# Optimization experiments

Hardware: AMD Instinct MI355X
Metric: run time of the kernel (lower is better)

The kernel has to match this reference:

```python
import jax, jax.numpy as jnp
import numpy as np

N, E, F, H = 50000, 800000, 256, 64


def setup_inputs() -> dict:
    key = jax.random.key(0)
    ks = jax.random.split(key, 6)
    x = jax.random.normal(ks[0], (N, F), jnp.float32)
    edge_index = jax.random.randint(ks[1], (2, E), 0, N)
    init = lambda k, shp, fan: jax.random.normal(k, shp, jnp.float32) / np.float32(np.sqrt(fan))
    W1l = init(ks[2], (F, H), F)
    b1l = jnp.zeros((H,), jnp.float32)
    W1r = init(ks[3], (F, H), F)
    W2l = init(ks[4], (H, H), H)
    b2l = jnp.zeros((H,), jnp.float32)
    W2r = init(ks[5], (H, H), H)
    return dict(x=x, edge_index=edge_index, W1l=W1l, b1l=b1l, W1r=W1r,
                W2l=W2l, b2l=b2l, W2r=W2r)


def _sage(x, src, dst, Wl, bl, Wr, n):
    # SAGEConv: out = mean_{j->i}(lin_l(x)_j) + lin_r(x)_i
    m = x @ Wl + bl                                   # [N, H]
    agg = jax.ops.segment_sum(m[src], dst, num_segments=n)
    deg = jax.ops.segment_sum(jnp.ones((src.shape[0],), x.dtype), dst, num_segments=n)
    agg = agg / jnp.maximum(deg, 1.0)[:, None]        # mean aggregation
    return agg + x @ Wr


def reference(x, edge_index, W1l, b1l, W1r, W2l, b2l, W2r):
    src, dst = edge_index[0], edge_index[1]
    n = x.shape[0]
    # 2-layer SAGE encoder (dropout=0, no residual for 2 layers)
    h = jax.nn.relu(_sage(x, src, dst, W1l, b1l, W1r, n))
    z = _sage(h, src, dst, W2l, b2l, W2r, n)
    # UnitNorm: replace all-zero rows with randn, then row-wise L2 normalize
    valid = jnp.sum(z != 0, axis=1, keepdims=True) > 0
    r = jax.random.normal(jax.random.key(42), z.shape, z.dtype)
    z = jnp.where(valid, z, r)
    z = z / jnp.sqrt(jnp.sum(z * z, axis=1, keepdims=True))
    # dot-product decode on observed edges + positive-edge BCE loss
    scores = jnp.sum(z[src] * z[dst], axis=-1)        # [E]
    loss = -jnp.mean(jax.nn.log_sigmoid(scores))
    return z, loss
```

## Files before the change

### kernel.cpp

```cpp
#include <hip/hip_runtime.h>

#define N_NODES 50000
#define N_EDGES 800000
#define F_IN    256
#define H_DIM   64
#define NB_SCAN ((N_NODES + 255) / 256)
#define TILE_A  4096
#define EPT     (TILE_A / 256)
#define MAXB    5632

typedef __attribute__((ext_vector_type(8))) short short8;
typedef __attribute__((ext_vector_type(4))) float floatx4;

__device__ __forceinline__ unsigned short f2bf(float f) {
  unsigned int u;
  __builtin_memcpy(&u, &f, 4);
  u += 0x7fffu + ((u >> 16) & 1u);
  return (unsigned short)(u >> 16);
}
__device__ __forceinline__ float bf2f(unsigned short s) {
  unsigned int v = ((unsigned int)s) << 16; float f; __builtin_memcpy(&f, &v, 4); return f;
}
__device__ __forceinline__ float bflo(unsigned int u) {
  unsigned int v = u << 16; float f; __builtin_memcpy(&f, &v, 4); return f;
}
__device__ __forceinline__ float bfhi(unsigned int u) {
  unsigned int v = u & 0xffff0000u; float f; __builtin_memcpy(&f, &v, 4); return f;
}

template<int K>
__device__ __forceinline__ void pack_body(int t, const float* __restrict__ Wl,
                                          const float* __restrict__ Wr,
                                          unsigned short* __restrict__ Wb)
{
  int lane = t & 63;
  int f    = t >> 6;
  int m    = f & 1;
  int c    = (f >> 1) & 3;
  int ks   = f >> 3;
  const float* W = m ? Wr : Wl;
  int quad = lane >> 4, l15 = lane & 15;
  int col = c * 16 + l15;
  unsigned short u[8];
#pragma unroll
  for (int j = 0; j < 8; ++j) {
    int k = ks * 32 + quad * 8 + j;
    u[j] = f2bf(W[k * H_DIM + col]);
  }
  uint4 v;
  __builtin_memcpy(&v, u, 16);
  ((uint4*)Wb)[t] = v;
}

__global__ __launch_bounds__(256) void pack_all_k(
    const float* __restrict__ W1l, const float* __restrict__ W1r,
    const float* __restrict__ W2l, const float* __restrict__ W2r,
    unsigned short* __restrict__ Wb1, unsigned short* __restrict__ Wb2,
    float* __restrict__ loss_slot, int* __restrict__ bcur)
{
  if (blockIdx.x == 0) {
    if (threadIdx.x == 0) loss_slot[0] = 0.f;
    if (threadIdx.x < NB_SCAN) bcur[threadIdx.x] = 0;
  }
  int b = blockIdx.x;
  if (b < 16) {
    pack_body<F_IN>(b * 256 + threadIdx.x, W1l, W1r, Wb1);
  } else {
    pack_body<H_DIM>((b - 16) * 256 + threadIdx.x, W2l, W2r, Wb2);
  }
}

template<int K, bool XBF16>
__global__ __launch_bounds__(256, 4) void gemm_mfma_k(
    const void* __restrict__ X_,
    const unsigned short* __restrict__ Wb,
    const float* __restrict__ bl,
    unsigned short* __restrict__ outl, unsigned short* __restrict__ outr)
{
  constexpr int KP = K + 8;
  __shared__ unsigned short xs[64 * KP];
  const int row0 = blockIdx.x * 64;
  if (XBF16) {
    const uint4* X = (const uint4*)X_;
    const int CH = K / 8;
    for (int i = threadIdx.x; i < 64 * CH; i += 256) {
      int r = i / CH, c = i % CH;
      int row = row0 + r;
      uint4 v = (row < N_NODES) ? X[(size_t)row * CH + c] : make_uint4(0, 0, 0, 0);
      *(uint4*)&xs[r * KP + c * 8] = v;
    }
  } else {
    const float4* X = (const float4*)X_;
    const int CH = K / 4;
    for (int i = threadIdx.x; i < 64 * CH; i += 256) {
      int r = i / CH, c = i % CH;
      int row = row0 + r;
      float4 v = (row < N_NODES) ? X[(size_t)row * CH + c]
                                 : make_float4(0.f, 0.f, 0.f, 0.f);
      unsigned int lo = (unsigned int)f2bf(v.x) | ((unsigned int)f2bf(v.y) << 16);
      unsigned int hi = (unsigned int)f2bf(v.z) | ((unsigned int)f2bf(v.w) << 16);
      *(uint2*)&xs[r * KP + c * 4] = make_uint2(lo, hi);
    }
  }
  __syncthreads();

  const int lane = threadIdx.x & 63;
  const int w    = threadIdx.x >> 6;
  const int quad = lane >> 4;
  const int l15  = lane & 15;
  const int rloc = w * 16 + l15;

  floatx4 accl[4], accr[4];
#pragma unroll
  for (int c = 0; c < 4; ++c) { accl[c] = (floatx4)0.f; accr[c] = (floatx4)0.f; }

  const uint4* wbase = (const uint4*)Wb;
#pragma unroll
  for (int ks = 0; ks < K / 32; ++ks) {
    short8 af = *(const short8*)&xs[rloc * KP + ks * 32 + quad * 8];
#pragma unroll
    for (int c = 0; c < 4; ++c) {
      uint4 rl = wbase[((ks * 4 + c) * 2 + 0) * 64 + lane];
      uint4 rr = wbase[((ks * 4 + c) * 2 + 1) * 64 + lane];
      short8 bfl, bfr;
      __builtin_memcpy(&bfl, &rl, 16);
      __builtin_memcpy(&bfr, &rr, 16);
      accl[c] = __builtin_amdgcn_mfma_f32_16x16x32_bf16(af, bfl, accl[c], 0, 0, 0);
      accr[c] = __builtin_amdgcn_mfma_f32_16x16x32_bf16(af, bfr, accr[c], 0, 0, 0);
    }
  }
#pragma unroll
  for (int c = 0; c < 4; ++c) {
    int col = c * 16 + l15;
    float bias = bl[col];
#pragma unroll
    for (int reg = 0; reg < 4; ++reg) {
      int row = row0 + w * 16 + quad * 4 + reg;
      if (row < N_NODES) {
        outl[(size_t)row * H_DIM + col] = f2bf(accl[c][reg] + bias);
        outr[(size_t)row * H_DIM + col] = f2bf(accr[c][reg]);
      }
    }
  }
}

__global__ __launch_bounds__(256) void binA_k(const int* __restrict__ ei,
                                              int* __restrict__ bcur,
                                              unsigned int* __restrict__ ebuf)
{
  __shared__ int lcnt[256];
  __shared__ int lofs[256];
  __shared__ int lstart[256];
  __shared__ int gstart[256];
  __shared__ int lcur[256];
  __shared__ unsigned int ldata[TILE_A];
  const int t = threadIdx.x;
  const int e0 = blockIdx.x * TILE_A;
  lcnt[t] = 0;
  __syncthreads();
  int ss[EPT], ds[EPT];
#pragma unroll
  for (int j = 0; j < EPT; ++j) {
    int e = e0 + t + j * 256;
    if (e < N_EDGES) {
      ss[j] = ei[e];
      ds[j] = ei[N_EDGES + e];
      atomicAdd(&lcnt[ds[j] >> 8], 1);
    } else {
      ds[j] = -1;
    }
  }
  __syncthreads();
  int v = lcnt[t];
  lofs[t] = v;
  __syncthreads();
  for (int off = 1; off < 256; off <<= 1) {
    int u = (t >= off) ? lofs[t - off] : 0;
    __syncthreads();
    lofs[t] += u;
    __syncthreads();
  }
  lstart[t] = lofs[t] - v;
  lcur[t]   = lofs[t] - v;
  if (t < NB_SCAN && v > 0) gstart[t] = atomicAdd(&bcur[t], v);
  __syncthreads();
#pragma unroll
  for (int j = 0; j < EPT; ++j) {
    if (ds[j] >= 0) {
      int p = atomicAdd(&lcur[ds[j] >> 8], 1);
      ldata[p] = ((unsigned int)ss[j] << 8) | (unsigned int)(ds[j] & 255);
    }
  }
  __syncthreads();
  int w = t >> 6, lane = t & 63;
  for (int b = w; b < NB_SCAN; b += 4) {
    int st = lstart[b], len = lcnt[b];
    if (len == 0) continue;
    int g = gstart[b];
    unsigned int* dst = ebuf + (size_t)b * MAXB;
    for (int j = lane; j < len; j += 64) {
      int gp = g + j;
      if (gp < MAXB) dst[gp] = ldata[st + j];
    }
  }
}

__global__ __launch_bounds__(256) void binB_k(const unsigned int* __restrict__ ebuf,
                                              const int* __restrict__ bcur,
                                              int* __restrict__ esrc,
                                              int* __restrict__ edst,
                                              int* __restrict__ rowptr)
{
  __shared__ int sc[256];
  __shared__ int ncnt[256];
  __shared__ int nscan[256];
  __shared__ int ncur[256];
  __shared__ int sh_se[2];
  __shared__ unsigned int sdata[MAXB];
  const int b = blockIdx.x, t = threadIdx.x;
  int bl = (t < NB_SCAN) ? min(bcur[t], MAXB) : 0;
  sc[t] = bl;
  __syncthreads();
  for (int off = 1; off < 256; off <<= 1) {
    int u = (t >= off) ? sc[t - off] : 0;
    __syncthreads();
    sc[t] += u;
    __syncthreads();
  }
  if (t == b) { sh_se[0] = sc[t] - bl; sh_se[1] = bl; }
  __syncthreads();
  const int start = sh_se[0], len = sh_se[1];
  const unsigned int* eb = ebuf + (size_t)b * MAXB;
  ncnt[t] = 0;
  __syncthreads();
  for (int i = t; i < len; i += 256) atomicAdd(&ncnt[eb[i] & 255], 1);
  __syncthreads();
  int v = ncnt[t];
  nscan[t] = v;
  __syncthreads();
  for (int off = 1; off < 256; off <<= 1) {
    int u = (t >= off) ? nscan[t - off] : 0;
    __syncthreads();
    nscan[t] += u;
    __syncthreads();
  }
  ncur[t] = nscan[t] - v;
  __syncthreads();
  for (int i = t; i < len; i += 256) {
    unsigned int e = eb[i];
    int p = atomicAdd(&ncur[e & 255], 1);
    sdata[p] = e >> 8;
  }
  __syncthreads();
  for (int i = t; i < len; i += 256) esrc[start + i] = (int)sdata[i];
  int node = b * 256 + t;
  int s0 = start + nscan[t] - v;
  if (node < N_NODES) {
    rowptr[node] = s0;
    if (node == N_NODES - 1) rowptr[N_NODES] = s0 + v;
  }
  for (int j = 0; j < v; ++j) edst[s0 + j] = node;
}

__device__ __forceinline__ float agg_row_b(const int* __restrict__ esrc,
                                           const unsigned short* __restrict__ m,
                                           int b, int e, int lane)
{
  float a0 = 0.f, a1 = 0.f, a2 = 0.f, a3 = 0.f;
  float a4 = 0.f, a5 = 0.f, a6 = 0.f, a7 = 0.f;
  int i = b;
  for (; i + 8 <= e; i += 8) {
    int s0 = esrc[i],     s1 = esrc[i + 1], s2 = esrc[i + 2], s3 = esrc[i + 3];
    int s4 = esrc[i + 4], s5 = esrc[i + 5], s6 = esrc[i + 6], s7 = esrc[i + 7];
    a0 += bf2f(m[(size_t)s0 * H_DIM + lane]);
    a1 += bf2f(m[(size_t)s1 * H_DIM + lane]);
    a2 += bf2f(m[(size_t)s2 * H_DIM + lane]);
    a3 += bf2f(m[(size_t)s3 * H_DIM + lane]);
    a4 += bf2f(m[(size_t)s4 * H_DIM + lane]);
    a5 += bf2f(m[(size_t)s5 * H_DIM + lane]);
    a6 += bf2f(m[(size_t)s6 * H_DIM + lane]);
    a7 += bf2f(m[(size_t)s7 * H_DIM + lane]);
  }
  for (; i + 4 <= e; i += 4) {
    int s0 = esrc[i], s1 = esrc[i + 1], s2 = esrc[i + 2], s3 = esrc[i + 3];
    a0 += bf2f(m[(size_t)s0 * H_DIM + lane]);
    a1 += bf2f(m[(size_t)s1 * H_DIM + lane]);
    a2 += bf2f(m[(size_t)s2 * H_DIM + lane]);
    a3 += bf2f(m[(size_t)s3 * H_DIM + lane]);
  }
  for (; i < e; ++i) a0 += bf2f(m[(size_t)esrc[i] * H_DIM + lane]);
  return ((a0 + a1) + (a2 + a3)) + ((a4 + a5) + (a6 + a7));
}

__global__ __launch_bounds__(256) void agg1_k(
    const int* __restrict__ rowptr, const int* __restrict__ esrc,
    const unsigned short* __restrict__ m, const unsigned short* __restrict__ xr,
    unsigned short* __restrict__ h)
{
  int gid = blockIdx.x * 256 + threadIdx.x;
  int row = gid >> 6, lane = gid & 63;
  if (row >= N_NODES) return;
  int b = rowptr[row], e = rowptr[row + 1];
  float acc = agg_row_b(esrc, m, b, e, lane);
  float dv = fmaxf((float)(e - b), 1.f);
  size_t o = (size_t)row * H_DIM + lane;
  h[o] = f2bf(fmaxf(acc / dv + bf2f(xr[o]), 0.f));
}

__global__ __launch_bounds__(256) void agg2_k(
    const int* __restrict__ rowptr, const int* __restrict__ esrc,
    const unsigned short* __restrict__ m, const unsigned short* __restrict__ hr,
    float* __restrict__ zout, unsigned short* __restrict__ zb)
{
  int gid = blockIdx.x * 256 + threadIdx.x;
  int row = gid >> 6, lane = gid & 63;
  if (row >= N_NODES) return;
  int b = rowptr[row], e = rowptr[row + 1];
  float acc = agg_row_b(esrc, m, b, e, lane);
  float dv = fmaxf((float)(e - b), 1.f);
  size_t o = (size_t)row * H_DIM + lane;
  float v = acc / dv + bf2f(hr[o]);
  float ss = v * v;
#pragma unroll
  for (int mm = 32; mm >= 1; mm >>= 1) ss += __shfl_xor(ss, mm, 64);
  float z = v * rsqrtf(fmaxf(ss, 1e-30f));
  zout[o] = z;
  zb[o] = f2bf(z);
}

__global__ __launch_bounds__(256) void decode2_k(
    const int* __restrict__ esrc, const int* __restrict__ edst,
    const unsigned short* __restrict__ zb, float* __restrict__ loss_slot)
{
  int i0 = (blockIdx.x * 256 + threadIdx.x) * 2;
  float part = 0.f;
  if (i0 + 1 < N_EDGES) {
    int s0 = esrc[i0],     d0 = edst[i0];
    int s1 = esrc[i0 + 1], d1 = edst[i0 + 1];
    const uint4* zs0 = (const uint4*)(zb + (size_t)s0 * H_DIM);
    const uint4* zd0 = (const uint4*)(zb + (size_t)d0 * H_DIM);
    const uint4* zs1 = (const uint4*)(zb + (size_t)s1 * H_DIM);
    const uint4* zd1 = (const uint4*)(zb + (size_t)d1 * H_DIM);
    float p0 = 0.f, p1 = 0.f;
#pragma unroll 4
    for (int k = 0; k < 8; ++k) {
      uint4 a0 = zs0[k], b0 = zd0[k], a1 = zs1[k], b1 = zd1[k];
      unsigned int au0[4] = {a0.x, a0.y, a0.z, a0.w};
      unsigned int bu0[4] = {b0.x, b0.y, b0.z, b0.w};
      unsigned int au1[4] = {a1.x, a1.y, a1.z, a1.w};
      unsigned int bu1[4] = {b1.x, b1.y, b1.z, b1.w};
#pragma unroll
      for (int j = 0; j < 4; ++j) {
        p0 = fmaf(bflo(au0[j]), bflo(bu0[j]), p0);
        p0 = fmaf(bfhi(au0[j]), bfhi(bu0[j]), p0);
        p1 = fmaf(bflo(au1[j]), bflo(bu1[j]), p1);
        p1 = fmaf(bfhi(au1[j]), bfhi(bu1[j]), p1);
      }
    }
    part  = fmaxf(-p0, 0.f) + log1pf(expf(-fabsf(p0)));
    part += fmaxf(-p1, 0.f) + log1pf(expf(-fabsf(p1)));
  }
#pragma unroll
  for (int m = 32; m >= 1; m >>= 1) part += __shfl_xor(part, m, 64);
  __shared__ float sbuf[4];
  int lane = threadIdx.x & 63, w = threadIdx.x >> 6;
  if (lane == 0) sbuf[w] = part;
  __syncthreads();
  if (threadIdx.x == 0)
    atomicAdd(loss_slot, (sbuf[0] + sbuf[1] + sbuf[2] + sbuf[3]) * (1.0f / N_EDGES));
}

extern "C" void kernel_launch(void* const* d_in, const int* in_sizes, int n_in,
                              void* d_out, int out_size, void* d_ws, size_t ws_size,
                              hipStream_t stream)
{
  (void)in_sizes; (void)n_in; (void)out_size; (void)ws_size;
  const float* x   = (const float*)d_in[0];
  const int*   ei  = (const int*)d_in[1];
  const float* W1l = (const float*)d_in[2];
  const float* b1l = (const float*)d_in[3];
  const float* W1r = (const float*)d_in[4];
  const float* W2l = (const float*)d_in[5];
  const float* b2l = (const float*)d_in[6];
  const float* W2r = (const float*)d_in[7];
  float* out = (float*)d_out;
  float* loss_slot = out + (size_t)N_NODES * H_DIM;

  const size_t NH = (size_t)N_NODES * H_DIM;
  unsigned short* uA = (unsigned short*)d_ws;
  unsigned short* uB = uA + NH;
  unsigned short* uC = uB + NH;
  unsigned short* Wb1 = uC + NH;
  unsigned short* Wb2 = Wb1 + (F_IN / 32) * 4 * 2 * 64 * 8;
  int* rowptr = (int*)(Wb2 + (H_DIM / 32) * 4 * 2 * 64 * 8);
  int* esrc   = rowptr + N_NODES + 1;
  int* edst   = esrc + N_EDGES;
  int* bcur   = edst + N_EDGES;
  unsigned int* ebuf = (unsigned int*)(bcur + NB_SCAN);

  dim3 blk(256);
  dim3 g_tile((N_NODES + 63) / 64);
  dim3 g_edge2((N_EDGES / 2 + 255) / 256);
  dim3 g_node((N_NODES * 64 + 255) / 256);
  dim3 g_binA((N_EDGES + TILE_A - 1) / TILE_A);
  dim3 g_bin(NB_SCAN);

  pack_all_k<<<dim3(20), blk, 0, stream>>>(W1l, W1r, W2l, W2r, Wb1, Wb2,
                                           loss_slot, bcur);
  binA_k<<<g_binA, blk, 0, stream>>>(ei, bcur, ebuf);
  binB_k<<<g_bin, blk, 0, stream>>>(ebuf, bcur, esrc, edst, rowptr);
  gemm_mfma_k<F_IN, false><<<g_tile, blk, 0, stream>>>(x, Wb1, b1l, uA, uC);
  agg1_k<<<g_node, blk, 0, stream>>>(rowptr, esrc, uA, uC, uB);
  gemm_mfma_k<H_DIM, true><<<g_tile, blk, 0, stream>>>(uB, Wb2, b2l, uA, uC);
  agg2_k<<<g_node, blk, 0, stream>>>(rowptr, esrc, uA, uC, out, uB);
  decode2_k<<<g_edge2, blk, 0, stream>>>(esrc, edst, uB, loss_slot);
}
```

Measured before the change: 254.5 us.

## Fuse binB into gemm1 launch and decode loss over CSR rows without edst

Merges the CSR bin-sort stage and the first-layer GEMM into one launch, with blocks split by index and sharing one shared-memory buffer, so the independent work overlaps and a launch is saved. The edge decode now walks CSR rows with one wavefront per destination node. Each destination row of z is loaded once per wavefront and every neighbour dot product is reduced with wave shuffles, which removes the edst array and its writes in binB. The trade-offs are per-edge shuffle reductions and load imbalance across rows of different degree in the decode. The fused kernel's shared-memory size follows the larger GEMM tile, which may limit occupancy for the binB blocks.

```diff
diff --git a/kernel.cpp b/kernel.cpp
--- a/kernel.cpp
+++ b/kernel.cpp
@@ -8,6 +8,8 @@
 #define TILE_A  4096
 #define EPT     (TILE_A / 256)
 #define MAXB    5632
+#define GT1     ((N_NODES + 63) / 64)
+#define DEC_BLOCKS 1568
 
 typedef __attribute__((ext_vector_type(8))) short short8;
 typedef __attribute__((ext_vector_type(4))) float floatx4;
@@ -20,12 +22,6 @@
 }
 __device__ __forceinline__ float bf2f(unsigned short s) {
   unsigned int v = ((unsigned int)s) << 16; float f; __builtin_memcpy(&f, &v, 4); return f;
-}
-__device__ __forceinline__ float bflo(unsigned int u) {
-  unsigned int v = u << 16; float f; __builtin_memcpy(&f, &v, 4); return f;
-}
-__device__ __forceinline__ float bfhi(unsigned int u) {
-  unsigned int v = u & 0xffff0000u; float f; __builtin_memcpy(&f, &v, 4); return f;
 }
 
 template<int K>
@@ -71,15 +67,15 @@
 }
 
 template<int K, bool XBF16>
-__global__ __launch_bounds__(256, 4) void gemm_mfma_k(
+__device__ __forceinline__ void gemm_body(
+    int bx, unsigned short* xs,
     const void* __restrict__ X_,
     const unsigned short* __restrict__ Wb,
     const float* __restrict__ bl,
     unsigned short* __restrict__ outl, unsigned short* __restrict__ outr)
 {
   constexpr int KP = K + 8;
-  __shared__ unsigned short xs[64 * KP];
-  const int row0 = blockIdx.x * 64;
+  const int row0 = bx * 64;
   if (XBF16) {
     const uint4* X = (const uint4*)X_;
     const int CH = K / 8;
@@ -205,19 +201,18 @@
   }
 }
 
-__global__ __launch_bounds__(256) void binB_k(const unsigned int* __restrict__ ebuf,
-                                              const int* __restrict__ bcur,
-                                              int* __restrict__ esrc,
-                                              int* __restrict__ edst,
-                                              int* __restrict__ rowptr)
-{
-  __shared__ int sc[256];
-  __shared__ int ncnt[256];
-  __shared__ int nscan[256];
-  __shared__ int ncur[256];
-  __shared__ int sh_se[2];
-  __shared__ unsigned int sdata[MAXB];
-  const int b = blockIdx.x, t = threadIdx.x;
+__device__ __forceinline__ void binB_body(
+    int b, unsigned char* smem,
+    const unsigned int* __restrict__ ebuf, const int* __restrict__ bcur,
+    int* __restrict__ esrc, int* __restrict__ rowptr)
+{
+  int* sc    = (int*)smem;
+  int* ncnt  = sc + 256;
+  int* nscan = ncnt + 256;
+  int* ncur  = nscan + 256;
+  int* sh_se = ncur + 256;
+  unsigned int* sdata = (unsigned int*)(sh_se + 2);
+  const int t = threadIdx.x;
   int bl = (t < NB_SCAN) ? min(bcur[t], MAXB) : 0;
   sc[t] = bl;
   __syncthreads();
@@ -259,7 +254,30 @@
     rowptr[node] = s0;
     if (node == N_NODES - 1) rowptr[N_NODES] = s0 + v;
   }
-  for (int j = 0; j < v; ++j) edst[s0 + j] = node;
+}
+
+__global__ __launch_bounds__(256, 4) void binB_gemm1_k(
+    const float* __restrict__ x, const unsigned short* __restrict__ Wb1,
+    const float* __restrict__ b1l,
+    unsigned short* __restrict__ m1, unsigned short* __restrict__ xr,
+    const unsigned int* __restrict__ ebuf, const int* __restrict__ bcur,
+    int* __restrict__ esrc, int* __restrict__ rowptr)
+{
+  __shared__ __align__(16) unsigned char smem[64 * (F_IN + 8) * 2];
+  if (blockIdx.x < GT1) {
+    gemm_body<F_IN, false>(blockIdx.x, (unsigned short*)smem, x, Wb1, b1l, m1, xr);
+  } else {
+    binB_body(blockIdx.x - GT1, smem, ebuf, bcur, esrc, rowptr);
+  }
+}
+
+__global__ __launch_bounds__(256, 4) void gemm2_k(
+    const void* __restrict__ X_, const unsigned short* __restrict__ Wb,
+    const float* __restrict__ bl,
+    unsigned short* __restrict__ outl, unsigned short* __restrict__ outr)
+{
+  __shared__ __align__(16) unsigned short xs[64 * (H_DIM + 8)];
+  gemm_body<H_DIM, true>(blockIdx.x, xs, X_, Wb, bl, outl, outr);
 }
 
 __device__ __forceinline__ float agg_row_b(const int* __restrict__ esrc,
@@ -328,42 +346,41 @@
   zb[o] = f2bf(z);
 }
 
-__global__ __launch_bounds__(256) void decode2_k(
-    const int* __restrict__ esrc, const int* __restrict__ edst,
+__global__ __launch_bounds__(256) void decode_csr_k(
+    const int* __restrict__ rowptr, const int* __restrict__ esrc,
     const unsigned short* __restrict__ zb, float* __restrict__ loss_slot)
 {
-  int i0 = (blockIdx.x * 256 + threadIdx.x) * 2;
+  const int lane = threadIdx.x & 63;
+  const int wid  = (blockIdx.x * 256 + threadIdx.x) >> 6;
+  const int nw   = DEC_BLOCKS * 4;
   float part = 0.f;
-  if (i0 + 1 < N_EDGES) {
-    int s0 = esrc[i0],     d0 = edst[i0];
-    int s1 = esrc[i0 + 1], d1 = edst[i0 + 1];
-    const uint4* zs0 = (const uint4*)(zb + (size_t)s0 * H_DIM);
-    const uint4* zd0 = (const uint4*)(zb + (size_t)d0 * H_DIM);
-    const uint4* zs1 = (const uint4*)(zb + (size_t)s1 * H_DIM);
-    const uint4* zd1 = (const uint4*)(zb + (size_t)d1 * H_DIM);
-    float p0 = 0.f, p1 = 0.f;
-#pragma unroll 4
-    for (int k = 0; k < 8; ++k) {
-      uint4 a0 = zs0[k], b0 = zd0[k], a1 = zs1[k], b1 = zd1[k];
-      unsigned int au0[4] = {a0.x, a0.y, a0.z, a0.w};
-      unsigned int bu0[4] = {b0.x, b0.y, b0.z, b0.w};
-      unsigned int au1[4] = {a1.x, a1.y, a1.z, a1.w};
-      unsigned int bu1[4] = {b1.x, b1.y, b1.z, b1.w};
-#pragma unroll
-      for (int j = 0; j < 4; ++j) {
-        p0 = fmaf(bflo(au0[j]), bflo(bu0[j]), p0);
-        p0 = fmaf(bfhi(au0[j]), bfhi(bu0[j]), p0);
-        p1 = fmaf(bflo(au1[j]), bflo(bu1[j]), p1);
-        p1 = fmaf(bfhi(au1[j]), bfhi(bu1[j]), p1);
+  for (int row = wid; row < N_NODES; row += nw) {
+    int b = rowptr[row], e = rowptr[row + 1];
+    if (b == e) continue;
+    float zd = bf2f(zb[(size_t)row * H_DIM + lane]);
+    int i = b;
+    for (; i + 2 <= e; i += 2) {
+      int s0 = esrc[i], s1 = esrc[i + 1];
+      float p0 = bf2f(zb[(size_t)s0 * H_DIM + lane]) * zd;
+      float p1 = bf2f(zb[(size_t)s1 * H_DIM + lane]) * zd;
+#pragma unroll
+      for (int m = 32; m >= 1; m >>= 1) {
+        p0 += __shfl_xor(p0, m, 64);
+        p1 += __shfl_xor(p1, m, 64);
       }
-    }
-    part  = fmaxf(-p0, 0.f) + log1pf(expf(-fabsf(p0)));
-    part += fmaxf(-p1, 0.f) + log1pf(expf(-fabsf(p1)));
-  }
-#pragma unroll
-  for (int m = 32; m >= 1; m >>= 1) part += __shfl_xor(part, m, 64);
+      part += fmaxf(-p0, 0.f) + log1pf(expf(-fabsf(p0)));
+      part += fmaxf(-p1, 0.f) + log1pf(expf(-fabsf(p1)));
+    }
+    if (i < e) {
+      int s = esrc[i];
+      float p = bf2f(zb[(size_t)s * H_DIM + lane]) * zd;
+#pragma unroll
+      for (int m = 32; m >= 1; m >>= 1) p += __shfl_xor(p, m, 64);
+      part += fmaxf(-p, 0.f) + log1pf(expf(-fabsf(p)));
+    }
+  }
   __shared__ float sbuf[4];
-  int lane = threadIdx.x & 63, w = threadIdx.x >> 6;
+  int w = threadIdx.x >> 6;
   if (lane == 0) sbuf[w] = part;
   __syncthreads();
   if (threadIdx.x == 0)
@@ -394,24 +411,23 @@
   unsigned short* Wb2 = Wb1 + (F_IN / 32) * 4 * 2 * 64 * 8;
   int* rowptr = (int*)(Wb2 + (H_DIM / 32) * 4 * 2 * 64 * 8);
   int* esrc   = rowptr + N_NODES + 1;
-  int* edst   = esrc + N_EDGES;
-  int* bcur   = edst + N_EDGES;
+  int* bcur   = esrc + N_EDGES;
   unsigned int* ebuf = (unsigned int*)(bcur + NB_SCAN);
 
   dim3 blk(256);
-  dim3 g_tile((N_NODES + 63) / 64);
-  dim3 g_edge2((N_EDGES / 2 + 255) / 256);
   dim3 g_node((N_NODES * 64 + 255) / 256);
   dim3 g_binA((N_EDGES + TILE_A - 1) / TILE_A);
-  dim3 g_bin(NB_SCAN);
+  dim3 g_fuse(GT1 + NB_SCAN);
+  dim3 g_tile(GT1);
+  dim3 g_dec(DEC_BLOCKS);
 
   pack_all_k<<<dim3(20), blk, 0, stream>>>(W1l, W1r, W2l, W2r, Wb1, Wb2,
                                            loss_slot, bcur);
   binA_k<<<g_binA, blk, 0, stream>>>(ei, bcur, ebuf);
-  binB_k<<<g_bin, blk, 0, stream>>>(ebuf, bcur, esrc, edst, rowptr);
-  gemm_mfma_k<F_IN, false><<<g_tile, blk, 0, stream>>>(x, Wb1, b1l, uA, uC);
+  binB_gemm1_k<<<g_fuse, blk, 0, stream>>>(x, Wb1, b1l, uA, uC,
+                                           ebuf, bcur, esrc, rowptr);
   agg1_k<<<g_node, blk, 0, stream>>>(rowptr, esrc, uA, uC, uB);
-  gemm_mfma_k<H_DIM, true><<<g_tile, blk, 0, stream>>>(uB, Wb2, b2l, uA, uC);
+  gemm2_k<<<g_tile, blk, 0, stream>>>(uB, Wb2, b2l, uA, uC);
   agg2_k<<<g_node, blk, 0, stream>>>(rowptr, esrc, uA, uC, out, uB);
-  decode2_k<<<g_edge2, blk, 0, stream>>>(esrc, edst, uB, loss_slot);
-}
+  decode_csr_k<<<g_dec, blk, 0, stream>>>(rowptr, esrc, uB, loss_slot);
+}
```

Result: slower. 413.9 us (+62.6%).
